# Performance work log

Measured on AMD Instinct MI355X. Metric: run time of the kernel, lower is better.

## Reference

```python
import jax, jax.numpy as jnp
import numpy as np

B, D = 8192, 256
NUM_CLASSES = 128
CHUNK = 256          # matches module chunk_size; B % CHUNK == 0
TEMP = 0.07
EPS_NORM = 1e-12


def setup_inputs() -> dict:
    key = jax.random.key(0)
    k1, k2 = jax.random.split(key)
    features = jax.random.normal(k1, (B, D), dtype=jnp.float32)
    labels = jax.random.randint(k2, (B,), 0, NUM_CLASSES, dtype=jnp.int64)
    return {"features": features, "labels": labels}


def reference(features, labels):
    n = features.shape[0]
    temperature = max(TEMP, 1e-4)

    # F.normalize(dim=1): x / max(||x||, eps)
    norm = jnp.maximum(jnp.linalg.norm(features, axis=1, keepdims=True), EPS_NORM)
    f = features / norm
    # clamp is a no-op after normalization but kept for faithfulness
    f = jnp.clip(f, -1000.0, 1000.0)

    # [B, B] similarity; the torch loop computes exactly these rows chunk by chunk
    sim = jnp.matmul(f, f.T) / temperature

    # self-mask: each row i masks column i (diagonal of its chunk's square block)
    self_mask = ~jnp.eye(n, dtype=bool)

    # positive mask: same label, excluding self
    pos = (labels[:, None] == labels[None, :]) & self_mask
    # per-chunk fallback: if a 256-row chunk has no positives at all, use self_mask
    pos_c = pos.reshape(n // CHUNK, CHUNK, n)
    has_pos = pos_c.any(axis=(1, 2), keepdims=True)
    pos = jnp.where(has_pos, pos_c, self_mask.reshape(n // CHUNK, CHUNK, n)).reshape(n, n)

    # max-subtract BEFORE self-masking (faithful: includes self-sim = 1/temp)
    sim_max = jnp.max(sim, axis=1, keepdims=True)
    logits = jnp.clip(sim - jax.lax.stop_gradient(sim_max), -1000.0, 1000.0)

    exp_sim = jnp.maximum(jnp.exp(logits), 1e-8) * self_mask
    log_sum_exp = jnp.log(jnp.sum(exp_sim, axis=1, keepdims=True) + 1e-8)
    log_prob = jnp.maximum(logits - log_sum_exp, -1000.0)

    pos_pairs = jnp.sum(pos, axis=1)                      # [B] int
    row_loss = -jnp.sum(pos * log_prob, axis=1)           # [B]
    valid = pos_pairs > 0
    row_loss = jnp.where(valid, row_loss / jnp.maximum(pos_pairs, 1).astype(row_loss.dtype), 0.0)

    total_loss = jnp.sum(row_loss)
    total_pairs = jnp.sum(valid).astype(jnp.float32)
    mean_loss = total_loss / (total_pairs + 1e-8)
    loss = mean_loss  # reduction == 'mean'
    return loss, total_pairs, mean_loss
```

## Files before the change

kernel.cpp:

```cpp
#include <hip/hip_runtime.h>
#include <hip/hip_bf16.h>
#include <type_traits>

#define NB 8192
#define DD 256
#define INV_T (1.0f/0.07f)
#define LOG2E 1.4426950408889634f
#define K1    (INV_T*LOG2E)
#define CEXP  6.2087204553847255e-7f
#define NSPLIT 8
#define BM 256
#define BN 64
#define CPS (NB/NSPLIT)
#define NITER (CPS/BN)
#define BUFB (BN*DD*2)

typedef __attribute__((ext_vector_type(8))) short s8v;
typedef __attribute__((ext_vector_type(4))) float f4v;
typedef unsigned int u32;
typedef unsigned short u16;

#define OFF_FB   0
#define OFF_SE   (4*1024*1024)
#define OFF_SP   (OFF_SE + NSPLIT*NB*4)
#define OFF_CL   (OFF_SP + NSPLIT*NB*4)
#define OFF_CV   (OFF_CL + 256)
#define OFF_CNT  (OFF_CV + 256)

__global__ void k_norm(const float* __restrict__ feat,
                       __hip_bfloat16* __restrict__ fb, int* __restrict__ cnt) {
    if (blockIdx.x == 0 && threadIdx.x == 0) *cnt = 0;
    const int t = threadIdx.x;
    const int w = t >> 6, l = t & 63;
    const int row = blockIdx.x * 4 + w;
    const float4 v = ((const float4*)feat)[row * 64 + l];
    float s = v.x * v.x + v.y * v.y + v.z * v.z + v.w * v.w;
    #pragma unroll
    for (int d = 32; d; d >>= 1) s += __shfl_xor(s, d, 64);
    const float scale = 1.0f / fmaxf(sqrtf(s), 1e-12f);
    __hip_bfloat16 h0 = __float2bfloat16(v.x * scale);
    __hip_bfloat16 h1 = __float2bfloat16(v.y * scale);
    __hip_bfloat16 h2 = __float2bfloat16(v.z * scale);
    __hip_bfloat16 h3 = __float2bfloat16(v.w * scale);
    ushort4 o;
    o.x = *(u16*)&h0; o.y = *(u16*)&h1; o.z = *(u16*)&h2; o.w = *(u16*)&h3;
    ((ushort4*)fb)[row * 64 + l] = o;
}

__launch_bounds__(512)
__global__ void k_main(const __hip_bfloat16* __restrict__ fb,
                       const int* __restrict__ lab,
                       float* __restrict__ SE, float* __restrict__ SP) {
    __shared__ __align__(16) char ldsB[2 * BUFB];
    __shared__ int ldsLab[CPS];
    const int tid = threadIdx.x;
    const int l = tid & 63;
    const int l15 = l & 15, lg = l >> 4;
    const int bid = blockIdx.x;
    const int sp = bid & 7, rb = bid >> 3;
    const int wbase = rb * BM + (tid >> 6) * 32;
    const int col0 = sp * CPS;

    ldsLab[tid]       = lab[col0 + tid];
    ldsLab[tid + 512] = lab[col0 + 512 + tid];

    s8v a[2][8];
    #pragma unroll
    for (int m = 0; m < 2; m++)
        #pragma unroll
        for (int kk = 0; kk < 8; kk++)
            a[m][kk] = *(const s8v*)(fb + (wbase + m * 16 + l15) * DD + kk * 32 + lg * 8);

    int labr[8];
    #pragma unroll
    for (int m = 0; m < 2; m++)
        #pragma unroll
        for (int r = 0; r < 4; r++)
            labr[m * 4 + r] = lab[wbase + m * 16 + lg * 4 + r];

    float sE[8], sPa[8];
    #pragma unroll
    for (int i = 0; i < 8; i++) { sE[i] = 0.f; sPa[i] = 0.f; }

    s8v st[4];
    auto load_tile = [&](int t) {
        const char* gsrc = (const char*)fb + (size_t)(col0 + t * BN) * (DD * 2);
        #pragma unroll
        for (int i = 0; i < 4; i++)
            st[i] = *(const s8v*)(gsrc + tid * 16 + i * 8192);
    };
    auto write_tile = [&](int bufoff) {
        #pragma unroll
        for (int i = 0; i < 4; i++) {
            const int x = tid * 16 + i * 8192;
            const int br = x >> 9, inrow = x & 511;
            *(s8v*)(ldsB + bufoff + (br * 512 | (inrow ^ ((br & 7) << 4)))) = st[i];
        }
    };

    auto run = [&](auto diagC) {
        constexpr bool DIAG = decltype(diagC)::value;
        load_tile(0);
        write_tile(0);
        __syncthreads();
        for (int t = 0; t < NITER; t++) {
            const int curoff = (t & 1) * BUFB;
            if (t + 1 < NITER) load_tile(t + 1);

            int lc[4];
            #pragma unroll
            for (int n = 0; n < 4; n++)
                lc[n] = ldsLab[t * BN + n * 16 + l15];

            f4v acc[2][4];
            #pragma unroll
            for (int m = 0; m < 2; m++)
                #pragma unroll
                for (int n = 0; n < 4; n++)
                    acc[m][n] = (f4v){0.f, 0.f, 0.f, 0.f};

            #pragma unroll
            for (int kk = 0; kk < 8; kk++) {
                s8v b0, b1;
                {
                    const int br0 = 0 * 16 + l15, br1 = 1 * 16 + l15;
                    b0 = *(const s8v*)(ldsB + curoff + ((br0 * 512 + kk * 64 + lg * 16) ^ ((br0 & 7) << 4)));
                    b1 = *(const s8v*)(ldsB + curoff + ((br1 * 512 + kk * 64 + lg * 16) ^ ((br1 & 7) << 4)));
                }
                acc[0][0] = __builtin_amdgcn_mfma_f32_16x16x32_bf16(a[0][kk], b0, acc[0][0], 0, 0, 0);
                acc[1][0] = __builtin_amdgcn_mfma_f32_16x16x32_bf16(a[1][kk], b0, acc[1][0], 0, 0, 0);
                acc[0][1] = __builtin_amdgcn_mfma_f32_16x16x32_bf16(a[0][kk], b1, acc[0][1], 0, 0, 0);
                acc[1][1] = __builtin_amdgcn_mfma_f32_16x16x32_bf16(a[1][kk], b1, acc[1][1], 0, 0, 0);
            }
            #pragma unroll
            for (int kk = 0; kk < 8; kk++) {
                s8v b2, b3;
                {
                    const int br2 = 2 * 16 + l15, br3 = 3 * 16 + l15;
                    b2 = *(const s8v*)(ldsB + curoff + ((br2 * 512 + kk * 64 + lg * 16) ^ ((br2 & 7) << 4)));
                    b3 = *(const s8v*)(ldsB + curoff + ((br3 * 512 + kk * 64 + lg * 16) ^ ((br3 & 7) << 4)));
                }
                acc[0][2] = __builtin_amdgcn_mfma_f32_16x16x32_bf16(a[0][kk], b2, acc[0][2], 0, 0, 0);
                acc[1][2] = __builtin_amdgcn_mfma_f32_16x16x32_bf16(a[1][kk], b2, acc[1][2], 0, 0, 0);
                acc[0][3] = __builtin_amdgcn_mfma_f32_16x16x32_bf16(a[0][kk], b3, acc[0][3], 0, 0, 0);
                acc[1][3] = __builtin_amdgcn_mfma_f32_16x16x32_bf16(a[1][kk], b3, acc[1][3], 0, 0, 0);
            }

            const int cb = col0 + t * BN;
            auto ep = [&](int n) {
                #pragma unroll
                for (int m = 0; m < 2; m++)
                    #pragma unroll
                    for (int r = 0; r < 4; r++) {
                        const int idx = m * 4 + r;
                        const float v = acc[m][n][r];
                        float e = exp2f(v * K1);
                        bool pos = (lc[n] == labr[idx]);
                        if (DIAG) {
                            const int row = wbase + m * 16 + lg * 4 + r;
                            const int col = cb + n * 16 + l15;
                            const bool nself = (row != col);
                            e = nself ? e : 0.f;
                            pos = pos && nself;
                        }
                        sE[idx] += e;
                        sPa[idx] += pos ? v : 0.f;
                    }
            };
            ep(0); ep(1);
            ep(2); ep(3);

            if (t + 1 < NITER) write_tile(curoff ^ BUFB);
            __syncthreads();
        }
    };
    if ((rb >> 2) == sp) run(std::true_type{}); else run(std::false_type{});

    #pragma unroll
    for (int idx = 0; idx < 8; idx++) {
        #pragma unroll
        for (int d = 1; d < 16; d <<= 1) {
            sE[idx]  += __shfl_xor(sE[idx], d, 16);
            sPa[idx] += __shfl_xor(sPa[idx], d, 16);
        }
    }
    if (l15 == 0) {
        #pragma unroll
        for (int idx = 0; idx < 8; idx++) {
            const int row = wbase + (idx >> 2) * 16 + lg * 4 + (idx & 3);
            SE[sp * NB + row] = sE[idx];
            SP[sp * NB + row] = sPa[idx];
        }
    }
}

__global__ void k_rows(const int* __restrict__ lab,
                       const float* __restrict__ SE, const float* __restrict__ SP,
                       float* __restrict__ CL, float* __restrict__ CV,
                       int* __restrict__ cnt, float* __restrict__ out) {
    __shared__ int h[128];
    const int t = threadIdx.x;
    if (t < 128) h[t] = 0;
    __syncthreads();
    #pragma unroll
    for (int i = 0; i < 32; i++)
        atomicAdd(&h[lab[t + i * 256]], 1);
    __syncthreads();

    const int row = blockIdx.x * 256 + t;
    float se = 0.f, spa = 0.f;
    #pragma unroll
    for (int s = 0; s < NSPLIT; s++) {
        se  += SE[s * NB + row];
        spa += SP[s * NB + row];
    }
    const int n = h[lab[row]] - 1;
    const float lse = logf(se * CEXP + 1e-8f);
    const bool valid = n > 0;
    float loss = valid ? (lse - (spa - (float)n) * INV_T / (float)n) : 0.f;
    float vf = valid ? 1.f : 0.f;
    #pragma unroll
    for (int d = 32; d; d >>= 1) { loss += __shfl_xor(loss, d, 64); vf += __shfl_xor(vf, d, 64); }
    __shared__ float pl[4], pv[4];
    __shared__ int isLast;
    if ((t & 63) == 0) { pl[t >> 6] = loss; pv[t >> 6] = vf; }
    __syncthreads();
    if (t == 0) {
        CL[blockIdx.x] = pl[0] + pl[1] + pl[2] + pl[3];
        CV[blockIdx.x] = pv[0] + pv[1] + pv[2] + pv[3];
        __threadfence();
        isLast = (atomicAdd(cnt, 1) == 31);
    }
    __syncthreads();
    if (isLast) {
        __threadfence();
        float lsum = (t < 32) ? CL[t] : 0.f;
        float vsum = (t < 32) ? CV[t] : 0.f;
        #pragma unroll
        for (int d = 32; d; d >>= 1) { lsum += __shfl_xor(lsum, d, 64); vsum += __shfl_xor(vsum, d, 64); }
        if (t == 0) {
            const float mean = lsum / (vsum + 1e-8f);
            out[0] = mean;
            out[1] = vsum;
            out[2] = mean;
        }
    }
}

extern "C" void kernel_launch(void* const* d_in, const int* in_sizes, int n_in,
                              void* d_out, int out_size, void* d_ws, size_t ws_size,
                              hipStream_t stream) {
    (void)in_sizes; (void)n_in; (void)out_size; (void)ws_size;
    const float* feat = (const float*)d_in[0];
    const int*   lab  = (const int*)d_in[1];
    char* ws = (char*)d_ws;
    __hip_bfloat16* fb = (__hip_bfloat16*)(ws + OFF_FB);
    float* SE = (float*)(ws + OFF_SE);
    float* SP = (float*)(ws + OFF_SP);
    float* CL = (float*)(ws + OFF_CL);
    float* CV = (float*)(ws + OFF_CV);
    int*   cnt = (int*)(ws + OFF_CNT);
    float* out = (float*)d_out;

    hipLaunchKernelGGL(k_norm, dim3(NB / 4), dim3(256), 0, stream, feat, fb, cnt);
    hipLaunchKernelGGL(k_main, dim3(NB / BM * NSPLIT), dim3(512), 0, stream, fb, lab, SE, SP);
    hipLaunchKernelGGL(k_rows, dim3(NB / 256), dim3(256), 0, stream, lab, SE, SP, CL, CV, cnt, out);
}
```

Measured before the change: 70.73 us.

## Use 4x2 wave tiling with direct global-to-LDS loads in main kernel

Reorganizes the 8 waves of each block into a 4x2 grid. Each wave now holds 64 rows of A in registers and computes 32 columns per tile, instead of 32 rows across all 64 columns. This halves the LDS B-fragment reads per MFMA. Tile staging switches from register round-trip loads and stores to global_load_lds, applying the swizzle on the global source address. Partial row sums from the two column-waves are combined through LDS before the store. The cost is higher register pressure (64 A VGPRs, 16+16 accumulators), with launch bounds requesting 2 blocks per CU.

```diff
diff --git a/kernel.cpp b/kernel.cpp
--- a/kernel.cpp
+++ b/kernel.cpp
@@ -47,137 +47,126 @@
     ((ushort4*)fb)[row * 64 + l] = o;
 }
 
-__launch_bounds__(512)
+__device__ __forceinline__ void gld16(const void* g, void* l) {
+    __builtin_amdgcn_global_load_lds((const __attribute__((address_space(1))) u32*)g,
+                                     (__attribute__((address_space(3))) u32*)l, 16, 0, 0);
+}
+
+__launch_bounds__(512, 2)
 __global__ void k_main(const __hip_bfloat16* __restrict__ fb,
                        const int* __restrict__ lab,
                        float* __restrict__ SE, float* __restrict__ SP) {
     __shared__ __align__(16) char ldsB[2 * BUFB];
     __shared__ int ldsLab[CPS];
+    __shared__ float ldsRE[2][BM];
+    __shared__ float ldsRP[2][BM];
     const int tid = threadIdx.x;
+    const int w = tid >> 6;
     const int l = tid & 63;
     const int l15 = l & 15, lg = l >> 4;
+    const int wm = w >> 1, wn = w & 1;
     const int bid = blockIdx.x;
     const int sp = bid & 7, rb = bid >> 3;
-    const int wbase = rb * BM + (tid >> 6) * 32;
+    const int row0 = rb * BM;
+    const int wbase = row0 + wm * 64;
     const int col0 = sp * CPS;
 
     ldsLab[tid]       = lab[col0 + tid];
     ldsLab[tid + 512] = lab[col0 + 512 + tid];
 
-    s8v a[2][8];
-    #pragma unroll
-    for (int m = 0; m < 2; m++)
+    s8v a[4][8];
+    #pragma unroll
+    for (int m = 0; m < 4; m++)
         #pragma unroll
         for (int kk = 0; kk < 8; kk++)
             a[m][kk] = *(const s8v*)(fb + (wbase + m * 16 + l15) * DD + kk * 32 + lg * 8);
 
-    int labr[8];
-    #pragma unroll
-    for (int m = 0; m < 2; m++)
+    int labr[16];
+    #pragma unroll
+    for (int m = 0; m < 4; m++)
         #pragma unroll
         for (int r = 0; r < 4; r++)
             labr[m * 4 + r] = lab[wbase + m * 16 + lg * 4 + r];
 
-    float sE[8], sPa[8];
-    #pragma unroll
-    for (int i = 0; i < 8; i++) { sE[i] = 0.f; sPa[i] = 0.f; }
-
-    s8v st[4];
-    auto load_tile = [&](int t) {
-        const char* gsrc = (const char*)fb + (size_t)(col0 + t * BN) * (DD * 2);
-        #pragma unroll
-        for (int i = 0; i < 4; i++)
-            st[i] = *(const s8v*)(gsrc + tid * 16 + i * 8192);
-    };
-    auto write_tile = [&](int bufoff) {
+    float sE[16], sPa[16];
+    #pragma unroll
+    for (int i = 0; i < 16; i++) { sE[i] = 0.f; sPa[i] = 0.f; }
+
+    auto stage = [&](int t, int bufoff) {
+        const char* gt = (const char*)fb + (size_t)(col0 + t * BN) * (DD * 2);
         #pragma unroll
         for (int i = 0; i < 4; i++) {
-            const int x = tid * 16 + i * 8192;
-            const int br = x >> 9, inrow = x & 511;
-            *(s8v*)(ldsB + bufoff + (br * 512 | (inrow ^ ((br & 7) << 4)))) = st[i];
+            const int x = i * 8192 + w * 1024 + (l << 4);
+            const int br = x >> 9;
+            const int inrow = x & 511;
+            gld16(gt + br * 512 + (inrow ^ ((br & 7) << 4)),
+                  ldsB + bufoff + i * 8192 + w * 1024);
         }
     };
 
     auto run = [&](auto diagC) {
         constexpr bool DIAG = decltype(diagC)::value;
-        load_tile(0);
-        write_tile(0);
+        stage(0, 0);
         __syncthreads();
         for (int t = 0; t < NITER; t++) {
             const int curoff = (t & 1) * BUFB;
-            if (t + 1 < NITER) load_tile(t + 1);
-
-            int lc[4];
+            if (t + 1 < NITER) stage(t + 1, curoff ^ BUFB);
+
+            const int lc0 = ldsLab[t * BN + wn * 32 + l15];
+            const int lc1 = ldsLab[t * BN + wn * 32 + 16 + l15];
+
+            f4v acc[4][2];
             #pragma unroll
-            for (int n = 0; n < 4; n++)
-                lc[n] = ldsLab[t * BN + n * 16 + l15];
-
-            f4v acc[2][4];
-            #pragma unroll
-            for (int m = 0; m < 2; m++)
-                #pragma unroll
-                for (int n = 0; n < 4; n++)
-                    acc[m][n] = (f4v){0.f, 0.f, 0.f, 0.f};
+            for (int m = 0; m < 4; m++) {
+                acc[m][0] = (f4v){0.f, 0.f, 0.f, 0.f};
+                acc[m][1] = (f4v){0.f, 0.f, 0.f, 0.f};
+            }
 
             #pragma unroll
             for (int kk = 0; kk < 8; kk++) {
-                s8v b0, b1;
-                {
-                    const int br0 = 0 * 16 + l15, br1 = 1 * 16 + l15;
-                    b0 = *(const s8v*)(ldsB + curoff + ((br0 * 512 + kk * 64 + lg * 16) ^ ((br0 & 7) << 4)));
-                    b1 = *(const s8v*)(ldsB + curoff + ((br1 * 512 + kk * 64 + lg * 16) ^ ((br1 & 7) << 4)));
-                }
-                acc[0][0] = __builtin_amdgcn_mfma_f32_16x16x32_bf16(a[0][kk], b0, acc[0][0], 0, 0, 0);
-                acc[1][0] = __builtin_amdgcn_mfma_f32_16x16x32_bf16(a[1][kk], b0, acc[1][0], 0, 0, 0);
-                acc[0][1] = __builtin_amdgcn_mfma_f32_16x16x32_bf16(a[0][kk], b1, acc[0][1], 0, 0, 0);
-                acc[1][1] = __builtin_amdgcn_mfma_f32_16x16x32_bf16(a[1][kk], b1, acc[1][1], 0, 0, 0);
+                const int br0 = wn * 32 + l15;
+                const int br1 = wn * 32 + 16 + l15;
+                s8v b0 = *(const s8v*)(ldsB + curoff + ((br0 * 512 + kk * 64 + lg * 16) ^ ((br0 & 7) << 4)));
+                s8v b1 = *(const s8v*)(ldsB + curoff + ((br1 * 512 + kk * 64 + lg * 16) ^ ((br1 & 7) << 4)));
+                #pragma unroll
+                for (int m = 0; m < 4; m++)
+                    acc[m][0] = __builtin_amdgcn_mfma_f32_16x16x32_bf16(a[m][kk], b0, acc[m][0], 0, 0, 0);
+                #pragma unroll
+                for (int m = 0; m < 4; m++)
+                    acc[m][1] = __builtin_amdgcn_mfma_f32_16x16x32_bf16(a[m][kk], b1, acc[m][1], 0, 0, 0);
             }
+
+            const int cb = col0 + t * BN;
             #pragma unroll
-            for (int kk = 0; kk < 8; kk++) {
-                s8v b2, b3;
-                {
-                    const int br2 = 2 * 16 + l15, br3 = 3 * 16 + l15;
-                    b2 = *(const s8v*)(ldsB + curoff + ((br2 * 512 + kk * 64 + lg * 16) ^ ((br2 & 7) << 4)));
-                    b3 = *(const s8v*)(ldsB + curoff + ((br3 * 512 + kk * 64 + lg * 16) ^ ((br3 & 7) << 4)));
-                }
-                acc[0][2] = __builtin_amdgcn_mfma_f32_16x16x32_bf16(a[0][kk], b2, acc[0][2], 0, 0, 0);
-                acc[1][2] = __builtin_amdgcn_mfma_f32_16x16x32_bf16(a[1][kk], b2, acc[1][2], 0, 0, 0);
-                acc[0][3] = __builtin_amdgcn_mfma_f32_16x16x32_bf16(a[0][kk], b3, acc[0][3], 0, 0, 0);
-                acc[1][3] = __builtin_amdgcn_mfma_f32_16x16x32_bf16(a[1][kk], b3, acc[1][3], 0, 0, 0);
-            }
-
-            const int cb = col0 + t * BN;
-            auto ep = [&](int n) {
+            for (int n = 0; n < 2; n++) {
+                const int lcn = n ? lc1 : lc0;
+                const int coln = cb + wn * 32 + n * 16 + l15;
                 #pragma unroll
-                for (int m = 0; m < 2; m++)
+                for (int m = 0; m < 4; m++)
                     #pragma unroll
                     for (int r = 0; r < 4; r++) {
                         const int idx = m * 4 + r;
                         const float v = acc[m][n][r];
                         float e = exp2f(v * K1);
-                        bool pos = (lc[n] == labr[idx]);
+                        bool pos = (lcn == labr[idx]);
                         if (DIAG) {
                             const int row = wbase + m * 16 + lg * 4 + r;
-                            const int col = cb + n * 16 + l15;
-                            const bool nself = (row != col);
+                            const bool nself = (row != coln);
                             e = nself ? e : 0.f;
                             pos = pos && nself;
                         }
                         sE[idx] += e;
                         sPa[idx] += pos ? v : 0.f;
                     }
-            };
-            ep(0); ep(1);
-            ep(2); ep(3);
-
-            if (t + 1 < NITER) write_tile(curoff ^ BUFB);
+            }
+
             __syncthreads();
         }
     };
     if ((rb >> 2) == sp) run(std::true_type{}); else run(std::false_type{});
 
     #pragma unroll
-    for (int idx = 0; idx < 8; idx++) {
+    for (int idx = 0; idx < 16; idx++) {
         #pragma unroll
         for (int d = 1; d < 16; d <<= 1) {
             sE[idx]  += __shfl_xor(sE[idx], d, 16);
@@ -186,11 +175,17 @@
     }
     if (l15 == 0) {
         #pragma unroll
-        for (int idx = 0; idx < 8; idx++) {
-            const int row = wbase + (idx >> 2) * 16 + lg * 4 + (idx & 3);
-            SE[sp * NB + row] = sE[idx];
-            SP[sp * NB + row] = sPa[idx];
-        }
+        for (int idx = 0; idx < 16; idx++) {
+            const int rowl = wm * 64 + (idx >> 2) * 16 + lg * 4 + (idx & 3);
+            ldsRE[wn][rowl] = sE[idx];
+            ldsRP[wn][rowl] = sPa[idx];
+        }
+    }
+    __syncthreads();
+    {
+        const int r = tid & 255;
+        if (tid < 256) SE[sp * NB + row0 + r] = ldsRE[0][r] + ldsRE[1][r];
+        else           SP[sp * NB + row0 + r] = ldsRP[0][r] + ldsRP[1][r];
     }
 }
 
```

After: 100.5 us. 1.42x slower.
